# Performance work log

Measured on AMD Instinct MI355X. Metric: run time of the kernel, lower is better.

Reference implementation:

```python
import jax, jax.numpy as jnp
import numpy as np

DIM = 576
HEADS = 8
AGENT = 49
GRID_SIZE = 5
ORDER = 3
BN_EPS = 1e-5


def _kan_grid():
    h = 2.0 / GRID_SIZE  # grid_range [-1, 1]
    return jnp.arange(-ORDER, GRID_SIZE + ORDER + 1, dtype=jnp.float32) * h - 1.0


def _bsplines(x, grid):
    # x: (M, in) -> (M, in, GRID_SIZE + ORDER) Cox-de Boor B-spline bases (efficient-kan)
    xe = x[..., None]
    b = ((xe >= grid[:-1]) & (xe < grid[1:])).astype(x.dtype)
    for k in range(1, ORDER + 1):
        b = ((xe - grid[:-(k + 1)]) / (grid[k:-1] - grid[:-(k + 1)]) * b[..., :-1]
             + (grid[k + 1:] - xe) / (grid[k + 1:] - grid[1:-k]) * b[..., 1:])
    return b


def setup_inputs() -> dict:
    key = jax.random.key(0)
    ks = jax.random.split(key, 16)
    b, H, W = 32, 28, 28
    n, c = H * W, DIM
    nrm = lambda k, shape, std=0.02: jax.random.normal(k, shape, jnp.float32) * std
    return {
        "x": jax.random.normal(ks[0], (b, n, c), jnp.float32),
        "H": H,
        "W": W,
        "Wq": nrm(ks[1], (c, c)),
        "Wkv": nrm(ks[2], (2 * c, c)),
        "an_bias": nrm(ks[3], (HEADS, AGENT, 7, 7)),
        "na_bias": nrm(ks[4], (HEADS, AGENT, 7, 7)),
        "ah_bias": nrm(ks[5], (1, HEADS, AGENT, H, 1)),
        "aw_bias": nrm(ks[6], (1, HEADS, AGENT, 1, W)),
        "ha_bias": nrm(ks[7], (1, HEADS, H, 1, AGENT)),
        "wa_bias": nrm(ks[8], (1, HEADS, 1, W, AGENT)),
        "dwc_w": nrm(ks[9], (c, 1, 3, 3), 0.1),
        "dwc_b": jnp.zeros((c,), jnp.float32),
        "bn_gamma": jnp.ones((c,), jnp.float32),
        "bn_beta": jnp.zeros((c,), jnp.float32),
        "bn_mean": jnp.zeros((c,), jnp.float32),
        "bn_var": jnp.ones((c,), jnp.float32),
        "base_weight": nrm(ks[10], (c, c)),
        "spline_weight": nrm(ks[11], (c, c, GRID_SIZE + ORDER)),
        "spline_scaler": jnp.ones((c, c), jnp.float32),
    }


def reference(x, H, W, Wq, Wkv, an_bias, na_bias, ah_bias, aw_bias, ha_bias, wa_bias,
              dwc_w, dwc_b, bn_gamma, bn_beta, bn_mean, bn_var,
              base_weight, spline_weight, spline_scaler):
    b, n, c = x.shape
    h, hd = HEADS, c // HEADS
    scale = hd ** -0.5
    q = x @ Wq.T                       # (b,n,c)
    kv = x @ Wkv.T                     # (b,n,2c)  (sr_ratio == 1)
    k, v = kv[..., :c], kv[..., c:]
    # agent tokens: AdaptiveAvgPool2d(28x28 -> 7x7) == exact 4x4 mean pooling
    p = int(AGENT ** 0.5)
    agent = q.reshape(b, p, H // p, p, W // p, c).mean(axis=(2, 4)).reshape(b, AGENT, c)
    qh = q.reshape(b, n, h, hd).transpose(0, 2, 1, 3)       # (b,h,n,hd)
    kh = k.reshape(b, n, h, hd).transpose(0, 2, 1, 3)
    vh = v.reshape(b, n, h, hd).transpose(0, 2, 1, 3)
    ah = agent.reshape(b, AGENT, h, hd).transpose(0, 2, 1, 3)  # (b,h,A,hd)
    # stage 1: agent tokens attend to k/v (bilinear-upsampled 7x7 bias + separable bias)
    pb1 = jax.image.resize(an_bias, (h, AGENT, H, W), "bilinear").reshape(1, h, AGENT, n)
    pb2 = (ah_bias + aw_bias).reshape(1, h, AGENT, n)
    agent_attn = jax.nn.softmax(jnp.einsum("bhad,bhnd->bhan", ah * scale, kh) + pb1 + pb2, axis=-1)
    agent_v = jnp.einsum("bhan,bhnd->bhad", agent_attn, vh)    # (b,h,A,hd)
    # stage 2: queries attend to agent tokens
    ab1 = jax.image.resize(na_bias, (h, AGENT, H, W), "bilinear").reshape(1, h, AGENT, n).transpose(0, 1, 3, 2)
    ab2 = (ha_bias + wa_bias).reshape(1, h, n, AGENT)
    q_attn = jax.nn.softmax(jnp.einsum("bhnd,bhad->bhna", qh * scale, ah) + ab1 + ab2, axis=-1)
    out = jnp.einsum("bhna,bhad->bhnd", q_attn, agent_v).transpose(0, 2, 1, 3).reshape(b, n, c)
    # depthwise-conv + BN(eval) + ReLU residual on v
    vimg = v.transpose(0, 2, 1).reshape(b, c, H, W)
    y = jax.lax.conv_general_dilated(vimg, dwc_w, (1, 1), "SAME",
                                     feature_group_count=c,
                                     dimension_numbers=("NCHW", "OIHW", "NCHW"))
    y = y + dwc_b[None, :, None, None]
    scale_bn = (bn_gamma / jnp.sqrt(bn_var + BN_EPS))[None, :, None, None]
    y = (y - bn_mean[None, :, None, None]) * scale_bn + bn_beta[None, :, None, None]
    y = jax.nn.relu(y).reshape(b, c, n).transpose(0, 2, 1)
    out = out + y
    # KANLinear projection: silu base branch + B-spline branch
    xf = out.reshape(b * n, c)
    bases = _bsplines(xf, _kan_grid())                           # (M, in, 8)
    scaled = spline_weight * spline_scaler[..., None]            # (out, in, 8)
    proj = jax.nn.silu(xf) @ base_weight.T + jnp.einsum("mik,oik->mo", bases, scaled)
    return proj.reshape(b, n, c)
```

## Files before the change

### kernel.cpp

```cpp
#include <hip/hip_runtime.h>
#include <hip/hip_bf16.h>
#include <math.h>

#define B_ 32
#define N_ 784
#define C_ 576
#define H_ 28
#define W_ 28
#define HEADS_ 8
#define HD_ 72
#define AGENT_ 49
#define M_ (B_ * N_)
#define KTOT_ 5184
#define QKVW_ 1728
#define SCALE_ 0.11785113019775793f

#define SWZ64(row, chunk) (((row) << 6) + ((((chunk) ^ ((row) & 7))) << 3))

typedef unsigned short ushort_t;
typedef __attribute__((ext_vector_type(8))) unsigned short u16x8;
typedef __attribute__((ext_vector_type(8))) __bf16 bf16x8;
typedef __attribute__((ext_vector_type(4))) float f32x4;
typedef __attribute__((ext_vector_type(4))) unsigned u32x4;

__device__ __forceinline__ ushort_t f2bf(float f) {
  union { float f; unsigned u; } v; v.f = f;
  unsigned r = v.u + 0x7fffu + ((v.u >> 16) & 1u);
  return (ushort_t)(r >> 16);
}
__device__ __forceinline__ float bf2f(ushort_t u) {
  union { unsigned u; float f; } v; v.u = ((unsigned)u) << 16;
  return v.f;
}
__device__ __forceinline__ unsigned pack2(float lo, float hi) {
  __bf16 a = (__bf16)lo, b = (__bf16)hi;
  unsigned short ua = __builtin_bit_cast(unsigned short, a);
  unsigned short ub = __builtin_bit_cast(unsigned short, b);
  return (unsigned)ua | ((unsigned)ub << 16);
}

__global__ __launch_bounds__(256) void convert_x_kernel(
    const float* __restrict__ x, ushort_t* __restrict__ xbf) {
  const int total8 = M_ * C_ / 8;
  for (int i = blockIdx.x * 256 + threadIdx.x; i < total8; i += gridDim.x * 256) {
    f32x4 a = *(const f32x4*)(x + i * 8);
    f32x4 b = *(const f32x4*)(x + i * 8 + 4);
    u16x8 o;
    o[0]=f2bf(a[0]); o[1]=f2bf(a[1]); o[2]=f2bf(a[2]); o[3]=f2bf(a[3]);
    o[4]=f2bf(b[0]); o[5]=f2bf(b[1]); o[6]=f2bf(b[2]); o[7]=f2bf(b[3]);
    *(u16x8*)(xbf + i * 8) = o;
  }
}

__global__ __launch_bounds__(256) void pack_w_kernel(
    const float* __restrict__ Wq, const float* __restrict__ Wkv,
    ushort_t* __restrict__ wbf) {
  int total = QKVW_ * C_;
  for (int i = blockIdx.x * 256 + threadIdx.x; i < total; i += gridDim.x * 256) {
    int j = i / C_, k = i % C_;
    float v = (j < C_) ? Wq[(size_t)j * C_ + k] : Wkv[(size_t)(j - C_) * C_ + k];
    wbf[i] = f2bf(v);
  }
}

__global__ __launch_bounds__(256) void pack_b_kernel(
    const float* __restrict__ base_w, const float* __restrict__ spline_w,
    const float* __restrict__ spline_s, ushort_t* __restrict__ bpackb) {
  int o = blockIdx.x;
  for (int j = threadIdx.x; j < KTOT_; j += 256) {
    float v;
    if (j < C_) {
      v = base_w[(size_t)o * C_ + j];
    } else {
      int jj = j - C_;
      int i = jj >> 3, kk = jj & 7;
      v = spline_w[((size_t)o * C_ + i) * 8 + kk] * spline_s[(size_t)o * C_ + i];
    }
    bpackb[(size_t)o * KTOT_ + j] = f2bf(v);
  }
}

__device__ __forceinline__ float bilerp7(const float* __restrict__ Bsrc, int y, int x) {
  float sy = y * 0.25f - 0.375f;
  float sx = x * 0.25f - 0.375f;
  float fy0 = floorf(sy), fx0 = floorf(sx);
  int y0 = (int)fy0, x0 = (int)fx0;
  float fy = sy - fy0, fx = sx - fx0;
  int y0c = min(6, max(0, y0)), y1c = min(6, max(0, y0 + 1));
  int x0c = min(6, max(0, x0)), x1c = min(6, max(0, x0 + 1));
  float v00 = Bsrc[y0c * 7 + x0c], v01 = Bsrc[y0c * 7 + x1c];
  float v10 = Bsrc[y1c * 7 + x0c], v11 = Bsrc[y1c * 7 + x1c];
  return (1.f - fy) * ((1.f - fx) * v00 + fx * v01)
       + fy * ((1.f - fx) * v10 + fx * v11);
}

__global__ __launch_bounds__(256) void bias_kernel(
    const float* __restrict__ an_bias, const float* __restrict__ na_bias,
    const float* __restrict__ ah_bias, const float* __restrict__ aw_bias,
    const float* __restrict__ ha_bias, const float* __restrict__ wa_bias,
    float* __restrict__ abias, float* __restrict__ qbias) {
  int idx = blockIdx.x * 256 + threadIdx.x;
  if (idx >= HEADS_ * AGENT_ * N_) return;
  int n = idx % N_;
  int ha = idx / N_;
  int h = ha / AGENT_, a = ha % AGENT_;
  int y = n / W_, x = n % W_;
  float pb1 = bilerp7(an_bias + (size_t)ha * 49, y, x);
  float pb2 = ah_bias[ha * H_ + y] + aw_bias[ha * W_ + x];
  abias[(size_t)ha * N_ + n] = pb1 + pb2;
  float ab1 = bilerp7(na_bias + (size_t)ha * 49, y, x);
  float ab2 = ha_bias[(h * H_ + y) * AGENT_ + a] + wa_bias[(h * W_ + x) * AGENT_ + a];
  qbias[((size_t)h * N_ + n) * AGENT_ + a] = ab1 + ab2;
}

__global__ __launch_bounds__(512, 4) void mfma_qkv_kernel(
    const ushort_t* __restrict__ A, const ushort_t* __restrict__ Bt,
    ushort_t* __restrict__ out) {
  __shared__ ushort_t Asl[2][128 * 64];
  __shared__ ushort_t Bsl[2][192 * 64];
  const int tid = threadIdx.x;
  const int lane = tid & 63, wid = tid >> 6;
  const int wm = wid >> 2, wn = wid & 3;
  const int l16 = lane & 15, lq = lane >> 4;

  int lin = blockIdx.x;
  const int q = 220, r = 4;
  int xcd = lin & 7;
  int wg = (xcd < r ? xcd * (q + 1) : r * (q + 1) + (xcd - r) * q) + (lin >> 3);
  const int m0 = (wg / 9) * 128, n0 = (wg % 9) * 192;

  const int srowi = tid >> 3;
  const int chk = tid & 7;

  const ushort_t* arow0 = A + (size_t)(m0 + srowi) * C_ + chk * 8;
  const ushort_t* arow1 = arow0 + (size_t)64 * C_;
  const ushort_t* brow0 = Bt + (size_t)(n0 + srowi) * C_ + chk * 8;
  const ushort_t* brow1 = brow0 + (size_t)64 * C_;
  const ushort_t* brow2 = brow0 + (size_t)128 * C_;

  const int aW0 = SWZ64(srowi, chk), aW1 = SWZ64(srowi + 64, chk);
  const int bW0 = SWZ64(srowi, chk), bW1 = SWZ64(srowi + 64, chk),
            bW2 = SWZ64(srowi + 128, chk);

  f32x4 acc[4][3] = {};
  u16x8 ar0, ar1, br0, br1, br2;

  ar0 = *(const u16x8*)(arow0);
  ar1 = *(const u16x8*)(arow1);
  br0 = *(const u16x8*)(brow0);
  br1 = *(const u16x8*)(brow1);
  br2 = *(const u16x8*)(brow2);
  *(u16x8*)&Asl[0][aW0] = ar0;
  *(u16x8*)&Asl[0][aW1] = ar1;
  *(u16x8*)&Bsl[0][bW0] = br0;
  *(u16x8*)&Bsl[0][bW1] = br1;
  *(u16x8*)&Bsl[0][bW2] = br2;
  ar0 = *(const u16x8*)(arow0 + 64);
  ar1 = *(const u16x8*)(arow1 + 64);
  br0 = *(const u16x8*)(brow0 + 64);
  br1 = *(const u16x8*)(brow1 + 64);
  br2 = *(const u16x8*)(brow2 + 64);
  __syncthreads();

  const int NSTEP = C_ / 64;
  for (int s = 0; s < NSTEP; ++s) {
    const int cur = s & 1;
    if (s + 1 < NSTEP) {
      const int nxt = cur ^ 1;
      *(u16x8*)&Asl[nxt][aW0] = ar0;
      *(u16x8*)&Asl[nxt][aW1] = ar1;
      *(u16x8*)&Bsl[nxt][bW0] = br0;
      *(u16x8*)&Bsl[nxt][bW1] = br1;
      *(u16x8*)&Bsl[nxt][bW2] = br2;
      if (s + 2 < NSTEP) {
        const int kl = (s + 2) * 64;
        ar0 = *(const u16x8*)(arow0 + kl);
        ar1 = *(const u16x8*)(arow1 + kl);
        br0 = *(const u16x8*)(brow0 + kl);
        br1 = *(const u16x8*)(brow1 + kl);
        br2 = *(const u16x8*)(brow2 + kl);
      }
    }
    #pragma unroll
    for (int ks = 0; ks < 2; ++ks) {
      bf16x8 af[4], bfr[3];
      #pragma unroll
      for (int fm = 0; fm < 4; ++fm)
        af[fm] = *(const bf16x8*)&Asl[cur][SWZ64(wm * 64 + fm * 16 + l16, ks * 4 + lq)];
      #pragma unroll
      for (int fn = 0; fn < 3; ++fn)
        bfr[fn] = *(const bf16x8*)&Bsl[cur][SWZ64(wn * 48 + fn * 16 + l16, ks * 4 + lq)];
      #pragma unroll
      for (int fm = 0; fm < 4; ++fm)
        #pragma unroll
        for (int fn = 0; fn < 3; ++fn)
          acc[fm][fn] = __builtin_amdgcn_mfma_f32_16x16x32_bf16(
              af[fm], bfr[fn], acc[fm][fn], 0, 0, 0);
    }
    __syncthreads();
  }
  #pragma unroll
  for (int fm = 0; fm < 4; ++fm) {
    #pragma unroll
    for (int fn = 0; fn < 3; ++fn) {
      int col = n0 + wn * 48 + fn * 16 + l16;
      #pragma unroll
      for (int r2 = 0; r2 < 4; ++r2) {
        int row = m0 + wm * 64 + fm * 16 + lq * 4 + r2;
        out[(size_t)row * QKVW_ + col] = f2bf(acc[fm][fn][r2]);
      }
    }
  }
}

__device__ __forceinline__ u32x4 basesPack(float xv) {
  float s = __fmaf_rn(xv, 2.5f, 5.5f);
  float tf = floorf(s);
  int t = (int)tf;
  float u = s - tf;
  float u2 = u * u, u3 = u2 * u, um = 1.f - u;
  float p0 = u3 * (1.f / 6.f);
  float p1 = __fmaf_rn(u3, -0.5f, __fmaf_rn(u2, 0.5f, __fmaf_rn(u, 0.5f, 1.f / 6.f)));
  float p2 = __fmaf_rn(u3, 0.5f, __fmaf_rn(u2, -1.f, 2.f / 3.f));
  float p3 = um * um * um * (1.f / 6.f);
  unsigned lo = pack2(p3, p2);
  unsigned hi = pack2(p1, p0);
  unsigned long long packed = ((unsigned long long)hi << 32) | (unsigned long long)lo;
  int sh = t - 3;
  int ba = sh << 4;
  unsigned long long shl_lo = packed << (ba & 63);
  unsigned long long shr_sp = packed >> ((64 - ba) & 63);
  unsigned long long shl_hi = packed << ((ba - 64) & 63);
  unsigned long long shr_ng = packed >> ((-ba) & 63);
  unsigned long long Olo = (sh < 0) ? shr_ng : ((sh < 4) ? shl_lo : 0ull);
  unsigned long long Ohi = (sh <= 0) ? 0ull : ((sh < 4) ? shr_sp : shl_hi);
  if (t < 0 || t > 10) { Olo = 0ull; Ohi = 0ull; }
  u32x4 o;
  o[0] = (unsigned)Olo; o[1] = (unsigned)(Olo >> 32);
  o[2] = (unsigned)Ohi; o[3] = (unsigned)(Ohi >> 32);
  return o;
}

__device__ __forceinline__ u32x4 siluPack(const float* xv) {
  u32x4 o;
  #pragma unroll
  for (int e = 0; e < 4; ++e) {
    float v0 = xv[2 * e], v1 = xv[2 * e + 1];
    float s0 = v0 / (1.f + __expf(-v0));
    float s1 = v1 / (1.f + __expf(-v1));
    o[e] = pack2(s0, s1);
  }
  return o;
}

__global__ __launch_bounds__(512, 4) void kan_mfma_kernel(
    const float* __restrict__ xf, const ushort_t* __restrict__ Bt,
    float* __restrict__ out) {
  __shared__ ushort_t Asl[2][128 * 64];
  __shared__ ushort_t Bsl[2][192 * 64];
  const int tid = threadIdx.x;
  const int lane = tid & 63, wid = tid >> 6;
  const int wm = wid >> 2, wn = wid & 3;
  const int l16 = lane & 15, lq = lane >> 4;

  int lin = blockIdx.x;
  const int q = 73, r = 4;
  int xcd = lin & 7;
  int wg = (xcd < r ? xcd * (q + 1) : r * (q + 1) + (xcd - r) * q) + (lin >> 3);
  const int m0 = (wg / 3) * 128, n0 = (wg % 3) * 192;

  const int srowi = tid >> 3;
  const int chk = tid & 7;

  const float* xfr0 = xf + (size_t)(m0 + srowi) * C_;
  const float* xfr1 = xfr0 + (size_t)64 * C_;
  const ushort_t* brow0 = Bt + (size_t)(n0 + srowi) * KTOT_ + chk * 8;
  const ushort_t* brow1 = brow0 + (size_t)64 * KTOT_;
  const ushort_t* brow2 = brow0 + (size_t)128 * KTOT_;

  const int aW0 = SWZ64(srowi, chk), aW1 = SWZ64(srowi + 64, chk);
  const int bW0 = SWZ64(srowi, chk), bW1 = SWZ64(srowi + 64, chk),
            bW2 = SWZ64(srowi + 128, chk);

  f32x4 acc[4][3] = {};
  float xv0[8], xv1[8];
  u16x8 br0, br1, br2;

  {
    f32x4 a = *(const f32x4*)(xfr0 + chk * 8);
    f32x4 b = *(const f32x4*)(xfr0 + chk * 8 + 4);
    xv0[0]=a[0]; xv0[1]=a[1]; xv0[2]=a[2]; xv0[3]=a[3];
    xv0[4]=b[0]; xv0[5]=b[1]; xv0[6]=b[2]; xv0[7]=b[3];
    f32x4 c = *(const f32x4*)(xfr1 + chk * 8);
    f32x4 d = *(const f32x4*)(xfr1 + chk * 8 + 4);
    xv1[0]=c[0]; xv1[1]=c[1]; xv1[2]=c[2]; xv1[3]=c[3];
    xv1[4]=d[0]; xv1[5]=d[1]; xv1[6]=d[2]; xv1[7]=d[3];
  }
  br0 = *(const u16x8*)(brow0);
  br1 = *(const u16x8*)(brow1);
  br2 = *(const u16x8*)(brow2);
  *(u32x4*)&Asl[0][aW0] = siluPack(xv0);
  *(u32x4*)&Asl[0][aW1] = siluPack(xv1);
  *(u16x8*)&Bsl[0][bW0] = br0;
  *(u16x8*)&Bsl[0][bW1] = br1;
  *(u16x8*)&Bsl[0][bW2] = br2;
  {
    f32x4 a = *(const f32x4*)(xfr0 + 64 + chk * 8);
    f32x4 b = *(const f32x4*)(xfr0 + 64 + chk * 8 + 4);
    xv0[0]=a[0]; xv0[1]=a[1]; xv0[2]=a[2]; xv0[3]=a[3];
    xv0[4]=b[0]; xv0[5]=b[1]; xv0[6]=b[2]; xv0[7]=b[3];
    f32x4 c = *(const f32x4*)(xfr1 + 64 + chk * 8);
    f32x4 d = *(const f32x4*)(xfr1 + 64 + chk * 8 + 4);
    xv1[0]=c[0]; xv1[1]=c[1]; xv1[2]=c[2]; xv1[3]=c[3];
    xv1[4]=d[0]; xv1[5]=d[1]; xv1[6]=d[2]; xv1[7]=d[3];
  }
  br0 = *(const u16x8*)(brow0 + 64);
  br1 = *(const u16x8*)(brow1 + 64);
  br2 = *(const u16x8*)(brow2 + 64);
  __syncthreads();

  const int NSTEP = KTOT_ / 64;
  for (int s = 0; s < NSTEP; ++s) {
    const int cur = s & 1;
    if (s + 1 < NSTEP) {
      const int nxt = cur ^ 1;
      const int kg = (s + 1) * 64;
      u32x4 a0, a1;
      if (kg < C_) { a0 = siluPack(xv0); a1 = siluPack(xv1); }
      else         { a0 = basesPack(xv0[0]); a1 = basesPack(xv1[0]); }
      *(u32x4*)&Asl[nxt][aW0] = a0;
      *(u32x4*)&Asl[nxt][aW1] = a1;
      *(u16x8*)&Bsl[nxt][bW0] = br0;
      *(u16x8*)&Bsl[nxt][bW1] = br1;
      *(u16x8*)&Bsl[nxt][bW2] = br2;
      if (s + 2 < NSTEP) {
        const int kl = (s + 2) * 64;
        if (kl < C_) {
          f32x4 a = *(const f32x4*)(xfr0 + kl + chk * 8);
          f32x4 b = *(const f32x4*)(xfr0 + kl + chk * 8 + 4);
          xv0[0]=a[0]; xv0[1]=a[1]; xv0[2]=a[2]; xv0[3]=a[3];
          xv0[4]=b[0]; xv0[5]=b[1]; xv0[6]=b[2]; xv0[7]=b[3];
          f32x4 c = *(const f32x4*)(xfr1 + kl + chk * 8);
          f32x4 d = *(const f32x4*)(xfr1 + kl + chk * 8 + 4);
          xv1[0]=c[0]; xv1[1]=c[1]; xv1[2]=c[2]; xv1[3]=c[3];
          xv1[4]=d[0]; xv1[5]=d[1]; xv1[6]=d[2]; xv1[7]=d[3];
        } else {
          int i0 = ((kl - C_) >> 3) + chk;
          xv0[0] = xfr0[i0];
          xv1[0] = xfr1[i0];
        }
        br0 = *(const u16x8*)(brow0 + kl);
        br1 = *(const u16x8*)(brow1 + kl);
        br2 = *(const u16x8*)(brow2 + kl);
      }
    }
    #pragma unroll
    for (int ks = 0; ks < 2; ++ks) {
      bf16x8 af[4], bfr[3];
      #pragma unroll
      for (int fm = 0; fm < 4; ++fm)
        af[fm] = *(const bf16x8*)&Asl[cur][SWZ64(wm * 64 + fm * 16 + l16, ks * 4 + lq)];
      #pragma unroll
      for (int fn = 0; fn < 3; ++fn)
        bfr[fn] = *(const bf16x8*)&Bsl[cur][SWZ64(wn * 48 + fn * 16 + l16, ks * 4 + lq)];
      #pragma unroll
      for (int fm = 0; fm < 4; ++fm)
        #pragma unroll
        for (int fn = 0; fn < 3; ++fn)
          acc[fm][fn] = __builtin_amdgcn_mfma_f32_16x16x32_bf16(
              af[fm], bfr[fn], acc[fm][fn], 0, 0, 0);
    }
    __syncthreads();
  }
  #pragma unroll
  for (int fm = 0; fm < 4; ++fm) {
    #pragma unroll
    for (int fn = 0; fn < 3; ++fn) {
      int col = n0 + wn * 48 + fn * 16 + l16;
      #pragma unroll
      for (int r2 = 0; r2 < 4; ++r2) {
        int row = m0 + wm * 64 + fm * 16 + lq * 4 + r2;
        out[(size_t)row * C_ + col] = acc[fm][fn][r2];
      }
    }
  }
}

__global__ __launch_bounds__(576) void agent_pool_kernel(
    const ushort_t* __restrict__ qkvb, float* __restrict__ agent) {
  int ba = blockIdx.x;
  int b = ba / AGENT_, a = ba % AGENT_;
  int ay = a / 7, ax = a % 7;
  int ch = threadIdx.x;
  float s = 0.f;
  #pragma unroll
  for (int i2 = 0; i2 < 4; ++i2)
    #pragma unroll
    for (int i4 = 0; i4 < 4; ++i4)
      s += bf2f(qkvb[((size_t)b * N_ + (ay * 4 + i2) * W_ + (ax * 4 + i4)) * QKVW_ + ch]);
  agent[(size_t)ba * C_ + ch] = s * 0.0625f;
}

#define AKS_ 104
#define VTS_ 136
__global__ __launch_bounds__(256) void agent_attn_mfma_kernel(
    const float* __restrict__ agent, const ushort_t* __restrict__ qkvb,
    const float* __restrict__ abias, float* __restrict__ agent_v) {
  __shared__ ushort_t A_lds[64 * AKS_];
  __shared__ ushort_t K_lds[112 * AKS_];
  __shared__ ushort_t Vt_lds[80 * VTS_];
  __shared__ ushort_t P_lds[4][16 * VTS_];
  const int tid = threadIdx.x;
  const int lane = tid & 63, wid = tid >> 6;
  const int l16 = lane & 15, lq = lane >> 4;
  const int b = blockIdx.x >> 3, h = blockIdx.x & 7;

  for (int i = tid; i < 64 * AKS_; i += 256) A_lds[i] = 0;
  for (int i = tid; i < 112 * 32; i += 256) {
    int r = i >> 5, cc = 72 + (i & 31);
    K_lds[r * AKS_ + cc] = 0;
  }
  for (int i = tid; i < 80 * VTS_; i += 256) Vt_lds[i] = 0;
  for (int i = tid; i < 4 * 16 * 24; i += 256) {
    int w = i / (16 * 24), rest = i % (16 * 24);
    int r = rest / 24, cc = 112 + rest % 24;
    P_lds[w][r * VTS_ + cc] = 0;
  }
  for (int i = tid; i < AGENT_ * HD_; i += 256) {
    int a = i / HD_, d = i % HD_;
    A_lds[a * AKS_ + d] = f2bf(agent[((size_t)b * AGENT_ + a) * C_ + h * HD_ + d]);
  }

  int srow[4], scol[4]; bool sval[4];
  #pragma unroll
  for (int i = 0; i < 4; ++i) {
    int idx = tid + i * 256;
    srow[i] = idx / 9; scol[i] = idx % 9;
    sval[i] = idx < 1008;
  }
  const ushort_t* kbase = qkvb + (size_t)b * N_ * QKVW_ + C_ + h * HD_;
  const ushort_t* vbase = qkvb + (size_t)b * N_ * QKVW_ + 2 * C_ + h * HD_;

  u16x8 kreg[4], vreg[4];
  #pragma unroll
  for (int i = 0; i < 4; ++i) {
    if (sval[i]) {
      kreg[i] = *(const u16x8*)(kbase + (size_t)srow[i] * QKVW_ + scol[i] * 8);
      vreg[i] = *(const u16x8*)(vbase + (size_t)srow[i] * QKVW_ + scol[i] * 8);
    }
  }
  #pragma unroll
  for (int i = 0; i < 4; ++i) {
    if (sval[i]) {
      *(u16x8*)&K_lds[srow[i] * AKS_ + scol[i] * 8] = kreg[i];
      #pragma unroll
      for (int e = 0; e < 8; ++e)
        Vt_lds[(scol[i] * 8 + e) * VTS_ + srow[i]] = vreg[i][e];
    }
  }
  __syncthreads();

  float m_r[4] = {-1e30f, -1e30f, -1e30f, -1e30f};
  float l_r[4] = {};
  f32x4 O[5] = {};
  const float* bias_base[4];
  #pragma unroll
  for (int r = 0; r < 4; ++r) {
    int a = wid * 16 + lq * 4 + r;
    a = min(a, AGENT_ - 1);
    bias_base[r] = abias + ((size_t)h * AGENT_ + a) * N_;
  }

  for (int c = 0; c < 7; ++c) {
    if (c < 6) {
      const size_t off = (size_t)(c + 1) * 112 * QKVW_;
      #pragma unroll
      for (int i = 0; i < 4; ++i) {
        if (sval[i]) {
          kreg[i] = *(const u16x8*)(kbase + off + (size_t)srow[i] * QKVW_ + scol[i] * 8);
          vreg[i] = *(const u16x8*)(vbase + off + (size_t)srow[i] * QKVW_ + scol[i] * 8);
        }
      }
    }
    f32x4 sacc[7] = {};
    #pragma unroll
    for (int ks = 0; ks < 3; ++ks) {
      bf16x8 af = *(const bf16x8*)&A_lds[(wid * 16 + l16) * AKS_ + ks * 32 + lq * 8];
      #pragma unroll
      for (int nt = 0; nt < 7; ++nt) {
        bf16x8 bf = *(const bf16x8*)&K_lds[(nt * 16 + l16) * AKS_ + ks * 32 + lq * 8];
        sacc[nt] = __builtin_amdgcn_mfma_f32_16x16x32_bf16(af, bf, sacc[nt], 0, 0, 0);
      }
    }
    float cmax[4] = {-1e30f, -1e30f, -1e30f, -1e30f};
    const int nb = c * 112 + l16;
    #pragma unroll
    for (int nt = 0; nt < 7; ++nt)
      #pragma unroll
      for (int r = 0; r < 4; ++r) {
        float lg = sacc[nt][r] * SCALE_ + bias_base[r][nb + nt * 16];
        sacc[nt][r] = lg;
        cmax[r] = fmaxf(cmax[r], lg);
      }
    #pragma unroll
    for (int off = 1; off < 16; off <<= 1)
      #pragma unroll
      for (int r = 0; r < 4; ++r)
        cmax[r] = fmaxf(cmax[r], __shfl_xor(cmax[r], off));
    float scl[4], rs[4];
    #pragma unroll
    for (int r = 0; r < 4; ++r) {
      float nm = fmaxf(m_r[r], cmax[r]);
      scl[r] = __expf(m_r[r] - nm);
      m_r[r] = nm;
      rs[r] = 0.f;
    }
    #pragma unroll
    for (int nt = 0; nt < 7; ++nt)
      #pragma unroll
      for (int r = 0; r < 4; ++r) {
        float p = __expf(sacc[nt][r] - m_r[r]);
        rs[r] += p;
        P_lds[wid][(lq * 4 + r) * VTS_ + nt * 16 + l16] = f2bf(p);
      }
    #pragma unroll
    for (int off = 1; off < 16; off <<= 1)
      #pragma unroll
      for (int r = 0; r < 4; ++r)
        rs[r] += __shfl_xor(rs[r], off);
    #pragma unroll
    for (int r = 0; r < 4; ++r) l_r[r] = l_r[r] * scl[r] + rs[r];
    #pragma unroll
    for (int nt = 0; nt < 5; ++nt)
      #pragma unroll
      for (int r = 0; r < 4; ++r) O[nt][r] *= scl[r];
    #pragma unroll
    for (int ks = 0; ks < 4; ++ks) {
      bf16x8 pf = *(const bf16x8*)&P_lds[wid][l16 * VTS_ + ks * 32 + lq * 8];
      #pragma unroll
      for (int nt = 0; nt < 5; ++nt) {
        bf16x8 vf = *(const bf16x8*)&Vt_lds[(nt * 16 + l16) * VTS_ + ks * 32 + lq * 8];
        O[nt] = __builtin_amdgcn_mfma_f32_16x16x32_bf16(pf, vf, O[nt], 0, 0, 0);
      }
    }
    __syncthreads();
    if (c < 6) {
      #pragma unroll
      for (int i = 0; i < 4; ++i) {
        if (sval[i]) {
          *(u16x8*)&K_lds[srow[i] * AKS_ + scol[i] * 8] = kreg[i];
          #pragma unroll
          for (int e = 0; e < 8; ++e)
            Vt_lds[(scol[i] * 8 + e) * VTS_ + srow[i]] = vreg[i][e];
        }
      }
      __syncthreads();
    }
  }
  float inv[4];
  #pragma unroll
  for (int r = 0; r < 4; ++r) inv[r] = 1.f / l_r[r];
  #pragma unroll
  for (int nt = 0; nt < 5; ++nt) {
    int d = nt * 16 + l16;
    if (d >= HD_) continue;
    #pragma unroll
    for (int r = 0; r < 4; ++r) {
      int a = wid * 16 + lq * 4 + r;
      if (a < AGENT_)
        agent_v[(((size_t)b * HEADS_ + h) * AGENT_ + a) * HD_ + d] = O[nt][r] * inv[r];
    }
  }
}

__global__ __launch_bounds__(256) void q_attn_kernel(
    const ushort_t* __restrict__ qkvb, const float* __restrict__ agent,
    const float* __restrict__ agent_v, const float* __restrict__ qbias,
    float* __restrict__ xf) {
  __shared__ float ag_t[HD_ * 52];
  __shared__ float av_t[HD_ * 52];
  const int tid = threadIdx.x;
  const int h = blockIdx.y, b = blockIdx.z;
  for (int t = tid; t < AGENT_ * HD_; t += 256) {
    int a = t / HD_, d = t % HD_;
    ag_t[d * 52 + a] = agent[((size_t)b * AGENT_ + a) * C_ + h * HD_ + d];
    av_t[d * 52 + a] = agent_v[(((size_t)b * HEADS_ + h) * AGENT_ + a) * HD_ + d];
  }
  __syncthreads();
  const int n = blockIdx.x * 256 + tid;
  if (n >= N_) return;
  const ushort_t* qp = qkvb + ((size_t)b * N_ + n) * QKVW_ + h * HD_;
  const float* qb = qbias + ((size_t)h * N_ + n) * AGENT_;
  float lg[AGENT_];
  #pragma unroll
  for (int a = 0; a < AGENT_; ++a) lg[a] = qb[a];
  for (int d = 0; d < HD_; ++d) {
    float qd = bf2f(qp[d]) * SCALE_;
    #pragma unroll
    for (int a = 0; a < AGENT_; ++a) lg[a] += qd * ag_t[d * 52 + a];
  }
  float mx = -1e30f;
  #pragma unroll
  for (int a = 0; a < AGENT_; ++a) mx = fmaxf(mx, lg[a]);
  float s = 0.f;
  #pragma unroll
  for (int a = 0; a < AGENT_; ++a) { lg[a] = __expf(lg[a] - mx); s += lg[a]; }
  float inv = 1.f / s;
  #pragma unroll
  for (int a = 0; a < AGENT_; ++a) lg[a] *= inv;
  float* op = xf + ((size_t)b * N_ + n) * C_ + h * HD_;
  for (int d = 0; d < HD_; ++d) {
    float acc = 0.f;
    #pragma unroll
    for (int a = 0; a < AGENT_; ++a) acc += lg[a] * av_t[d * 52 + a];
    op[d] = acc;
  }
}

__global__ __launch_bounds__(288) void dwc_kernel(
    const ushort_t* __restrict__ qkvb, const float* __restrict__ w,
    const float* __restrict__ bias, const float* __restrict__ gamma,
    const float* __restrict__ beta, const float* __restrict__ mean,
    const float* __restrict__ var, float* __restrict__ xf) {
  int lin = blockIdx.x;
  const int bn = (lin & 7) * 3136 + (lin >> 3);
  const int b = bn / N_, n = bn % N_;
  const int y = n / W_, x = n % W_;
  const int c0 = threadIdx.x * 2;
  float a0 = 0.f, a1 = 0.f;
  #pragma unroll
  for (int ky = 0; ky < 3; ++ky) {
    int yy = y + ky - 1;
    if (yy < 0 || yy >= H_) continue;
    #pragma unroll
    for (int kx = 0; kx < 3; ++kx) {
      int xx = x + kx - 1;
      if (xx < 0 || xx >= W_) continue;
      unsigned v = *(const unsigned*)(qkvb + ((size_t)b * N_ + yy * W_ + xx) * QKVW_ + 2 * C_ + c0);
      a0 += w[c0 * 9 + ky * 3 + kx] * bf2f((ushort_t)(v & 0xffffu));
      a1 += w[(c0 + 1) * 9 + ky * 3 + kx] * bf2f((ushort_t)(v >> 16));
    }
  }
  float s0 = gamma[c0] * rsqrtf(var[c0] + 1e-5f);
  float s1 = gamma[c0 + 1] * rsqrtf(var[c0 + 1] + 1e-5f);
  float r0 = fmaxf((a0 + bias[c0] - mean[c0]) * s0 + beta[c0], 0.f);
  float r1 = fmaxf((a1 + bias[c0 + 1] - mean[c0 + 1]) * s1 + beta[c0 + 1], 0.f);
  float2* xp = (float2*)&xf[(size_t)bn * C_ + c0];
  float2 old = *xp;
  old.x += r0; old.y += r1;
  *xp = old;
}

extern "C" void kernel_launch(void* const* d_in, const int* in_sizes, int n_in,
                              void* d_out, int out_size, void* d_ws, size_t ws_size,
                              hipStream_t stream) {
  const float* x        = (const float*)d_in[0];
  const float* Wq       = (const float*)d_in[3];
  const float* Wkv      = (const float*)d_in[4];
  const float* an_bias  = (const float*)d_in[5];
  const float* na_bias  = (const float*)d_in[6];
  const float* ah_bias  = (const float*)d_in[7];
  const float* aw_bias  = (const float*)d_in[8];
  const float* ha_bias  = (const float*)d_in[9];
  const float* wa_bias  = (const float*)d_in[10];
  const float* dwc_w    = (const float*)d_in[11];
  const float* dwc_b    = (const float*)d_in[12];
  const float* bn_gamma = (const float*)d_in[13];
  const float* bn_beta  = (const float*)d_in[14];
  const float* bn_mean  = (const float*)d_in[15];
  const float* bn_var   = (const float*)d_in[16];
  const float* base_w   = (const float*)d_in[17];
  const float* spline_w = (const float*)d_in[18];
  const float* spline_s = (const float*)d_in[19];

  char* ws = (char*)d_ws;
  ushort_t* qkvb   = (ushort_t*)(ws + 0);
  ushort_t* xbf    = (ushort_t*)(ws + 86704128);
  ushort_t* wbf    = (ushort_t*)(ws + 115605504);
  ushort_t* bpackb = (ushort_t*)(ws + 117596160);
  float* agent     = (float*)(ws + 123568128);
  float* agent_v   = (float*)(ws + 127180800);
  float* abias     = (float*)(ws + 130793472);
  float* qbias     = (float*)(ws + 132022784);
  float* xf        = (float*)(ws + 133252096);
  float* out       = (float*)d_out;

  convert_x_kernel<<<dim3(2048), dim3(256), 0, stream>>>(x, xbf);
  pack_w_kernel<<<dim3(1024), dim3(256), 0, stream>>>(Wq, Wkv, wbf);
  pack_b_kernel<<<dim3(C_), dim3(256), 0, stream>>>(base_w, spline_w, spline_s, bpackb);
  bias_kernel<<<dim3((HEADS_ * AGENT_ * N_ + 255) / 256), dim3(256), 0, stream>>>(
      an_bias, na_bias, ah_bias, aw_bias, ha_bias, wa_bias, abias, qbias);
  mfma_qkv_kernel<<<dim3(1764), dim3(512), 0, stream>>>(xbf, wbf, qkvb);
  agent_pool_kernel<<<dim3(B_ * AGENT_), dim3(C_), 0, stream>>>(qkvb, agent);
  agent_attn_mfma_kernel<<<dim3(B_ * HEADS_), dim3(256), 0, stream>>>(
      agent, qkvb, abias, agent_v);
  q_attn_kernel<<<dim3(4, HEADS_, B_), dim3(256), 0, stream>>>(
      qkvb, agent, agent_v, qbias, xf);
  dwc_kernel<<<dim3(M_), dim3(288), 0, stream>>>(
      qkvb, dwc_w, dwc_b, bn_gamma, bn_beta, bn_mean, bn_var, xf);
  kan_mfma_kernel<<<dim3(588), dim3(512), 0, stream>>>(xf, bpackb, out);
}
```

Baseline: 618.2 us.

## Pre-tile swizzled bf16 operands and stream GEMM tiles via global_load_lds

```diff
diff --git a/kernel.cpp b/kernel.cpp
--- a/kernel.cpp
+++ b/kernel.cpp
@@ -38,45 +38,78 @@
   unsigned short ub = __builtin_bit_cast(unsigned short, b);
   return (unsigned)ua | ((unsigned)ub << 16);
 }
+__device__ __forceinline__ void gload16(const ushort_t* g, ushort_t* l) {
+  __builtin_amdgcn_global_load_lds(
+      (const __attribute__((address_space(1))) unsigned*)g,
+      (__attribute__((address_space(3))) unsigned*)l, 16, 0, 0);
+}
+
+__device__ __forceinline__ u16x8 packf8(f32x4 a, f32x4 b) {
+  u16x8 o;
+  o[0]=f2bf(a[0]); o[1]=f2bf(a[1]); o[2]=f2bf(a[2]); o[3]=f2bf(a[3]);
+  o[4]=f2bf(b[0]); o[5]=f2bf(b[1]); o[6]=f2bf(b[2]); o[7]=f2bf(b[3]);
+  return o;
+}
 
 __global__ __launch_bounds__(256) void convert_x_kernel(
-    const float* __restrict__ x, ushort_t* __restrict__ xbf) {
-  const int total8 = M_ * C_ / 8;
-  for (int i = blockIdx.x * 256 + threadIdx.x; i < total8; i += gridDim.x * 256) {
-    f32x4 a = *(const f32x4*)(x + i * 8);
-    f32x4 b = *(const f32x4*)(x + i * 8 + 4);
-    u16x8 o;
-    o[0]=f2bf(a[0]); o[1]=f2bf(a[1]); o[2]=f2bf(a[2]); o[3]=f2bf(a[3]);
-    o[4]=f2bf(b[0]); o[5]=f2bf(b[1]); o[6]=f2bf(b[2]); o[7]=f2bf(b[3]);
-    *(u16x8*)(xbf + i * 8) = o;
+    const float* __restrict__ x, ushort_t* __restrict__ xbt) {
+  const int totalg = 196 * 9 * 1024;
+  for (int g = blockIdx.x * 256 + threadIdx.x; g < totalg; g += gridDim.x * 256) {
+    int tile = g >> 10, gi = g & 1023;
+    int r = gi >> 3, chp = gi & 7;
+    int ch = chp ^ (r & 7);
+    int row = (tile / 9) * 128 + r;
+    int k0 = (tile % 9) * 64 + ch * 8;
+    const float* xp = x + (size_t)row * C_ + k0;
+    f32x4 a = *(const f32x4*)xp;
+    f32x4 b = *(const f32x4*)(xp + 4);
+    *(u16x8*)(xbt + (size_t)tile * 8192 + gi * 8) = packf8(a, b);
   }
 }
 
 __global__ __launch_bounds__(256) void pack_w_kernel(
     const float* __restrict__ Wq, const float* __restrict__ Wkv,
-    ushort_t* __restrict__ wbf) {
-  int total = QKVW_ * C_;
-  for (int i = blockIdx.x * 256 + threadIdx.x; i < total; i += gridDim.x * 256) {
-    int j = i / C_, k = i % C_;
-    float v = (j < C_) ? Wq[(size_t)j * C_ + k] : Wkv[(size_t)(j - C_) * C_ + k];
-    wbf[i] = f2bf(v);
+    ushort_t* __restrict__ wbt) {
+  int tile = blockIdx.x;
+  int nt = tile / 9, kw = tile % 9;
+  for (int gi = threadIdx.x; gi < 1536; gi += 256) {
+    int r = gi >> 3, chp = gi & 7;
+    int ch = chp ^ (r & 7);
+    int j = nt * 192 + r;
+    int k0 = kw * 64 + ch * 8;
+    const float* wp = (j < C_) ? (Wq + (size_t)j * C_ + k0)
+                               : (Wkv + (size_t)(j - C_) * C_ + k0);
+    f32x4 a = *(const f32x4*)wp;
+    f32x4 b = *(const f32x4*)(wp + 4);
+    *(u16x8*)(wbt + (size_t)tile * 12288 + gi * 8) = packf8(a, b);
   }
 }
 
 __global__ __launch_bounds__(256) void pack_b_kernel(
     const float* __restrict__ base_w, const float* __restrict__ spline_w,
-    const float* __restrict__ spline_s, ushort_t* __restrict__ bpackb) {
-  int o = blockIdx.x;
-  for (int j = threadIdx.x; j < KTOT_; j += 256) {
-    float v;
-    if (j < C_) {
-      v = base_w[(size_t)o * C_ + j];
+    const float* __restrict__ spline_s, ushort_t* __restrict__ btk) {
+  int tile = blockIdx.x;
+  int nt = tile / 81, kw = tile % 81;
+  for (int gi = threadIdx.x; gi < 1536; gi += 256) {
+    int r = gi >> 3, chp = gi & 7;
+    int ch = chp ^ (r & 7);
+    int o = nt * 192 + r;
+    int k0 = kw * 64 + ch * 8;
+    f32x4 a, b;
+    if (k0 < C_) {
+      const float* bp = base_w + (size_t)o * C_ + k0;
+      a = *(const f32x4*)bp;
+      b = *(const f32x4*)(bp + 4);
     } else {
-      int jj = j - C_;
-      int i = jj >> 3, kk = jj & 7;
-      v = spline_w[((size_t)o * C_ + i) * 8 + kk] * spline_s[(size_t)o * C_ + i];
-    }
-    bpackb[(size_t)o * KTOT_ + j] = f2bf(v);
+      int i = (k0 - C_) >> 3;
+      float sc = spline_s[(size_t)o * C_ + i];
+      const float* sp = spline_w + ((size_t)o * C_ + i) * 8;
+      a = *(const f32x4*)sp;
+      b = *(const f32x4*)(sp + 4);
+      a[0]*=sc; a[1]*=sc; a[2]*=sc; a[3]*=sc;
+      b[0]*=sc; b[1]*=sc; b[2]*=sc; b[3]*=sc;
+    }
+    *(u16x8*)(btk + (size_t)tile * 12288 + gi * 8) = packf8(a, b);
   }
 }
 
@@ -114,7 +147,7 @@
 }
 
 __global__ __launch_bounds__(512, 4) void mfma_qkv_kernel(
-    const ushort_t* __restrict__ A, const ushort_t* __restrict__ Bt,
+    const ushort_t* __restrict__ At, const ushort_t* __restrict__ Bt,
     ushort_t* __restrict__ out) {
   __shared__ ushort_t Asl[2][128 * 64];
   __shared__ ushort_t Bsl[2][192 * 64];
@@ -129,57 +162,33 @@
   int wg = (xcd < r ? xcd * (q + 1) : r * (q + 1) + (xcd - r) * q) + (lin >> 3);
   const int m0 = (wg / 9) * 128, n0 = (wg % 9) * 192;
 
-  const int srowi = tid >> 3;
-  const int chk = tid & 7;
-
-  const ushort_t* arow0 = A + (size_t)(m0 + srowi) * C_ + chk * 8;
-  const ushort_t* arow1 = arow0 + (size_t)64 * C_;
-  const ushort_t* brow0 = Bt + (size_t)(n0 + srowi) * C_ + chk * 8;
-  const ushort_t* brow1 = brow0 + (size_t)64 * C_;
-  const ushort_t* brow2 = brow0 + (size_t)128 * C_;
-
-  const int aW0 = SWZ64(srowi, chk), aW1 = SWZ64(srowi + 64, chk);
-  const int bW0 = SWZ64(srowi, chk), bW1 = SWZ64(srowi + 64, chk),
-            bW2 = SWZ64(srowi + 128, chk);
+  const ushort_t* aimg = At + (size_t)(wg / 9) * 9 * 8192;
+  const ushort_t* bimg = Bt + (size_t)(wg % 9) * 9 * 12288;
+  const int aslot = wid * 2;
+  const int bslot = wid * 3;
+
+  #pragma unroll
+  for (int u = 0; u < 2; ++u)
+    gload16(aimg + (size_t)(aslot + u) * 512 + lane * 8, &Asl[0][(aslot + u) * 512]);
+  #pragma unroll
+  for (int u = 0; u < 3; ++u)
+    gload16(bimg + (size_t)(bslot + u) * 512 + lane * 8, &Bsl[0][(bslot + u) * 512]);
+  __syncthreads();
 
   f32x4 acc[4][3] = {};
-  u16x8 ar0, ar1, br0, br1, br2;
-
-  ar0 = *(const u16x8*)(arow0);
-  ar1 = *(const u16x8*)(arow1);
-  br0 = *(const u16x8*)(brow0);
-  br1 = *(const u16x8*)(brow1);
-  br2 = *(const u16x8*)(brow2);
-  *(u16x8*)&Asl[0][aW0] = ar0;
-  *(u16x8*)&Asl[0][aW1] = ar1;
-  *(u16x8*)&Bsl[0][bW0] = br0;
-  *(u16x8*)&Bsl[0][bW1] = br1;
-  *(u16x8*)&Bsl[0][bW2] = br2;
-  ar0 = *(const u16x8*)(arow0 + 64);
-  ar1 = *(const u16x8*)(arow1 + 64);
-  br0 = *(const u16x8*)(brow0 + 64);
-  br1 = *(const u16x8*)(brow1 + 64);
-  br2 = *(const u16x8*)(brow2 + 64);
-  __syncthreads();
-
   const int NSTEP = C_ / 64;
   for (int s = 0; s < NSTEP; ++s) {
     const int cur = s & 1;
     if (s + 1 < NSTEP) {
       const int nxt = cur ^ 1;
-      *(u16x8*)&Asl[nxt][aW0] = ar0;
-      *(u16x8*)&Asl[nxt][aW1] = ar1;
-      *(u16x8*)&Bsl[nxt][bW0] = br0;
-      *(u16x8*)&Bsl[nxt][bW1] = br1;
-      *(u16x8*)&Bsl[nxt][bW2] = br2;
-      if (s + 2 < NSTEP) {
-        const int kl = (s + 2) * 64;
-        ar0 = *(const u16x8*)(arow0 + kl);
-        ar1 = *(const u16x8*)(arow1 + kl);
-        br0 = *(const u16x8*)(brow0 + kl);
-        br1 = *(const u16x8*)(brow1 + kl);
-        br2 = *(const u16x8*)(brow2 + kl);
-      }
+      const ushort_t* ai = aimg + (size_t)(s + 1) * 8192;
+      const ushort_t* bi = bimg + (size_t)(s + 1) * 12288;
+      #pragma unroll
+      for (int u = 0; u < 2; ++u)
+        gload16(ai + (size_t)(aslot + u) * 512 + lane * 8, &Asl[nxt][(aslot + u) * 512]);
+      #pragma unroll
+      for (int u = 0; u < 3; ++u)
+        gload16(bi + (size_t)(bslot + u) * 512 + lane * 8, &Bsl[nxt][(bslot + u) * 512]);
     }
     #pragma unroll
     for (int ks = 0; ks < 2; ++ks) {
@@ -274,18 +283,17 @@
 
   const float* xfr0 = xf + (size_t)(m0 + srowi) * C_;
   const float* xfr1 = xfr0 + (size_t)64 * C_;
-  const ushort_t* brow0 = Bt + (size_t)(n0 + srowi) * KTOT_ + chk * 8;
-  const ushort_t* brow1 = brow0 + (size_t)64 * KTOT_;
-  const ushort_t* brow2 = brow0 + (size_t)128 * KTOT_;
+  const ushort_t* bimg = Bt + (size_t)(wg % 3) * 81 * 12288;
+  const int bslot = wid * 3;
 
   const int aW0 = SWZ64(srowi, chk), aW1 = SWZ64(srowi + 64, chk);
-  const int bW0 = SWZ64(srowi, chk), bW1 = SWZ64(srowi + 64, chk),
-            bW2 = SWZ64(srowi + 128, chk);
 
   f32x4 acc[4][3] = {};
   float xv0[8], xv1[8];
-  u16x8 br0, br1, br2;
-
+
+  #pragma unroll
+  for (int u = 0; u < 3; ++u)
+    gload16(bimg + (size_t)(bslot + u) * 512 + lane * 8, &Bsl[0][(bslot + u) * 512]);
   {
     f32x4 a = *(const f32x4*)(xfr0 + chk * 8);
     f32x4 b = *(const f32x4*)(xfr0 + chk * 8 + 4);
@@ -296,14 +304,8 @@
     xv1[0]=c[0]; xv1[1]=c[1]; xv1[2]=c[2]; xv1[3]=c[3];
     xv1[4]=d[0]; xv1[5]=d[1]; xv1[6]=d[2]; xv1[7]=d[3];
   }
-  br0 = *(const u16x8*)(brow0);
-  br1 = *(const u16x8*)(brow1);
-  br2 = *(const u16x8*)(brow2);
   *(u32x4*)&Asl[0][aW0] = siluPack(xv0);
   *(u32x4*)&Asl[0][aW1] = siluPack(xv1);
-  *(u16x8*)&Bsl[0][bW0] = br0;
-  *(u16x8*)&Bsl[0][bW1] = br1;
-  *(u16x8*)&Bsl[0][bW2] = br2;
   {
     f32x4 a = *(const f32x4*)(xfr0 + 64 + chk * 8);
     f32x4 b = *(const f32x4*)(xfr0 + 64 + chk * 8 + 4);
@@ -314,9 +316,6 @@
     xv1[0]=c[0]; xv1[1]=c[1]; xv1[2]=c[2]; xv1[3]=c[3];
     xv1[4]=d[0]; xv1[5]=d[1]; xv1[6]=d[2]; xv1[7]=d[3];
   }
-  br0 = *(const u16x8*)(brow0 + 64);
-  br1 = *(const u16x8*)(brow1 + 64);
-  br2 = *(const u16x8*)(brow2 + 64);
   __syncthreads();
 
   const int NSTEP = KTOT_ / 64;
@@ -324,15 +323,16 @@
     const int cur = s & 1;
     if (s + 1 < NSTEP) {
       const int nxt = cur ^ 1;
+      const ushort_t* bi = bimg + (size_t)(s + 1) * 12288;
+      #pragma unroll
+      for (int u = 0; u < 3; ++u)
+        gload16(bi + (size_t)(bslot + u) * 512 + lane * 8, &Bsl[nxt][(bslot + u) * 512]);
       const int kg = (s + 1) * 64;
       u32x4 a0, a1;
       if (kg < C_) { a0 = siluPack(xv0); a1 = siluPack(xv1); }
       else         { a0 = basesPack(xv0[0]); a1 = basesPack(xv1[0]); }
       *(u32x4*)&Asl[nxt][aW0] = a0;
       *(u32x4*)&Asl[nxt][aW1] = a1;
-      *(u16x8*)&Bsl[nxt][bW0] = br0;
-      *(u16x8*)&Bsl[nxt][bW1] = br1;
-      *(u16x8*)&Bsl[nxt][bW2] = br2;
       if (s + 2 < NSTEP) {
         const int kl = (s + 2) * 64;
         if (kl < C_) {
@@ -349,9 +349,6 @@
           xv0[0] = xfr0[i0];
           xv1[0] = xfr1[i0];
         }
-        br0 = *(const u16x8*)(brow0 + kl);
-        br1 = *(const u16x8*)(brow1 + kl);
-        br2 = *(const u16x8*)(brow2 + kl);
       }
     }
     #pragma unroll
@@ -675,9 +672,9 @@
 
   char* ws = (char*)d_ws;
   ushort_t* qkvb   = (ushort_t*)(ws + 0);
-  ushort_t* xbf    = (ushort_t*)(ws + 86704128);
-  ushort_t* wbf    = (ushort_t*)(ws + 115605504);
-  ushort_t* bpackb = (ushort_t*)(ws + 117596160);
+  ushort_t* xbt    = (ushort_t*)(ws + 86704128);
+  ushort_t* wbt    = (ushort_t*)(ws + 115605504);
+  ushort_t* btk    = (ushort_t*)(ws + 117596160);
   float* agent     = (float*)(ws + 123568128);
   float* agent_v   = (float*)(ws + 127180800);
   float* abias     = (float*)(ws + 130793472);
@@ -685,12 +682,12 @@
   float* xf        = (float*)(ws + 133252096);
   float* out       = (float*)d_out;
 
-  convert_x_kernel<<<dim3(2048), dim3(256), 0, stream>>>(x, xbf);
-  pack_w_kernel<<<dim3(1024), dim3(256), 0, stream>>>(Wq, Wkv, wbf);
-  pack_b_kernel<<<dim3(C_), dim3(256), 0, stream>>>(base_w, spline_w, spline_s, bpackb);
+  convert_x_kernel<<<dim3(2048), dim3(256), 0, stream>>>(x, xbt);
+  pack_w_kernel<<<dim3(81), dim3(256), 0, stream>>>(Wq, Wkv, wbt);
+  pack_b_kernel<<<dim3(243), dim3(256), 0, stream>>>(base_w, spline_w, spline_s, btk);
   bias_kernel<<<dim3((HEADS_ * AGENT_ * N_ + 255) / 256), dim3(256), 0, stream>>>(
       an_bias, na_bias, ah_bias, aw_bias, ha_bias, wa_bias, abias, qbias);
-  mfma_qkv_kernel<<<dim3(1764), dim3(512), 0, stream>>>(xbf, wbf, qkvb);
+  mfma_qkv_kernel<<<dim3(1764), dim3(512), 0, stream>>>(xbt, wbt, qkvb);
   agent_pool_kernel<<<dim3(B_ * AGENT_), dim3(C_), 0, stream>>>(qkvb, agent);
   agent_attn_mfma_kernel<<<dim3(B_ * HEADS_), dim3(256), 0, stream>>>(
       agent, qkvb, abias, agent_v);
@@ -698,5 +695,5 @@
       qkvb, agent, agent_v, qbias, xf);
   dwc_kernel<<<dim3(M_), dim3(288), 0, stream>>>(
       qkvb, dwc_w, dwc_b, bn_gamma, bn_beta, bn_mean, bn_var, xf);
-  kan_mfma_kernel<<<dim3(588), dim3(512), 0, stream>>>(xf, bpackb, out);
-}
+  kan_mfma_kernel<<<dim3(588), dim3(512), 0, stream>>>(xf, btk, out);
+}
```

New measurement: 640.7 us. 3.6% more time.
